# Performance work log

Hardware: AMD Instinct MI355X
Metric: run time of the kernel (lower is better)

## Reference

```python
import jax, jax.numpy as jnp
import numpy as np

B, F, S = 8, 4000, 512   # batch, input_size, seq_len
E = H = 128              # embedding_size == hidden_size (linearlist applied to embedded nodes)
TOPK = 8
USE_MASK = True
EPS = 1e-4


def setup_inputs() -> dict:
    key = jax.random.key(0)
    k1, k2, k3, k4, k5 = jax.random.split(key, 5)
    be = 1.0 / np.sqrt(E)
    bh = 1.0 / np.sqrt(H)
    inputs = jax.random.uniform(k1, (B, F, S), dtype=jnp.float32)
    embedding = jax.random.uniform(k2, (F, E), minval=-be, maxval=be, dtype=jnp.float32)
    # stacked nn.ModuleList of seq_len Linear(hidden_size, seq_len) layers
    W = jax.random.uniform(k3, (S, H, S), minval=-bh, maxval=bh, dtype=jnp.float32)
    b = jax.random.uniform(k4, (S, S), minval=-bh, maxval=bh, dtype=jnp.float32)
    offset_prob = jax.random.uniform(k5, (1,), dtype=jnp.float32)  # unused by forward
    return {"inputs": inputs, "embedding": embedding, "W": W, "b": b, "offset_prob": offset_prob}


def _probs(inputs, embedding, W, b):
    # GraphEmbedding: tanh(inputs[:, :, i]^T @ embedding) for each node i -> [B,S,E]
    embedded = jnp.tanh(jnp.einsum('bfs,fe->bse', inputs, embedding))
    # per-node linear: logits[b, i, :] = embedded[b, i, :] @ W[i] + b[i]
    logits = jnp.einsum('bih,iho->bio', embedded, W) + b[None]
    return jnp.clip(jax.nn.sigmoid(logits), EPS, 1.0 - EPS)  # [B,S,S], == prev_probs


def _select_and_mask(probs):
    """Sequential per-node edge sampling + acyclic (transitive-closure) mask update.

    mask[b, a, c] == True  <=>  a is an ancestor of c in the DAG built so far.
    Vectorized equivalent of compute_mask/mask propagation in the torch source.
    """
    keys = jax.random.split(jax.random.key(42), S)
    batch_ix = jnp.arange(B)[:, None]

    def step(mask, xs):
        idx, key, p = xs  # p: [B, S] probabilities for node idx's parents
        samp = jax.random.bernoulli(key, p)  # [B, S] bool
        if TOPK != 0:
            _, top_ids = jax.lax.top_k(p, TOPK)
            keep = jnp.zeros((B, S), bool).at[batch_ix, top_ids].set(True)
            samp = samp & keep
        if USE_MASK:
            # apply_mask_to_actions: cannot pick a descendant of idx as parent
            samp = samp & ~mask[:, idx, :]
        samp = samp.at[:, idx].set(False)  # no self loop
        if USE_MASK:
            # compute_mask: add edges j->idx for selected j, keep transitive closure
            anc_of_sel = jnp.any(mask & samp[:, None, :], axis=-1)   # ancestors of any selected j
            col = mask[:, :, idx] | samp | anc_of_sel                # new ancestors of idx
            mask = mask.at[:, :, idx].set(col)
            row = mask[:, idx, :]                                    # descendants of idx
            mask = mask | (col[:, :, None] & row[:, None, :])        # anc(idx) x desc(idx)
        return mask, samp

    mask0 = jnp.zeros((B, S, S), bool)
    p_steps = jnp.transpose(probs, (1, 0, 2))  # [S, B, S]
    mask, rows = jax.lax.scan(step, mask0, (jnp.arange(S), keys, p_steps))
    prev_idxs = jnp.transpose(rows, (1, 0, 2))  # [B, S, S]
    return prev_idxs, mask


def reference(inputs, embedding, W, b, offset_prob):
    prev_probs = _probs(inputs, embedding, W, b)
    prev_idxs, mask = _select_and_mask(prev_probs)
    prev_probs_2 = jnp.zeros_like(prev_probs)  # never written in the torch forward
    return prev_probs, prev_probs_2, prev_idxs, mask
```

## Files before the change

kernel.cpp:

```cpp
#include <hip/hip_runtime.h>
#include <stdint.h>

#define S_    512
#define B_    8
#define F_    4000
#define E_    128
#define H_    128
#define TOPK_ 8
#define S2_   (S_*S_)
#define BSS_  (B_*S2_)
#define BSE_  (B_*S_*E_)
#define NCHUNK_ 8
typedef unsigned long long ull;

__device__ __forceinline__ void tf2x32(uint32_t k0, uint32_t k1, uint32_t& x0, uint32_t& x1) {
  uint32_t k2 = k0 ^ k1 ^ 0x1BD11BDAu;
  x0 += k0; x1 += k1;
#define TFR(r) { x0 += x1; x1 = (x1 << (r)) | (x1 >> (32 - (r))); x1 ^= x0; }
  TFR(13) TFR(15) TFR(26) TFR(6)
  x0 += k1; x1 += k2 + 1u;
  TFR(17) TFR(29) TFR(16) TFR(24)
  x0 += k2; x1 += k0 + 2u;
  TFR(13) TFR(15) TFR(26) TFR(6)
  x0 += k0; x1 += k1 + 3u;
  TFR(17) TFR(29) TFR(16) TFR(24)
  x0 += k1; x1 += k2 + 4u;
  TFR(13) TFR(15) TFR(26) TFR(6)
  x0 += k2; x1 += k0 + 5u;
#undef TFR
}

__device__ __forceinline__ void splitkey(int i, uint32_t& k0, uint32_t& k1) {
  uint32_t x0 = 0u, x1 = (uint32_t)i;
  tf2x32(0u, 42u, x0, x1);
  k0 = x0; k1 = x1;
}
__device__ __forceinline__ uint32_t randbits32(uint32_t k0, uint32_t k1, uint32_t m) {
  uint32_t x0 = 0u, x1 = m;
  tf2x32(k0, k1, x0, x1);
  return x0 ^ x1;
}

__global__ __launch_bounds__(256) void embed_kernel(const float* __restrict__ inputs,
                                                    const float* __restrict__ embedding,
                                                    double* __restrict__ part) {
  const int c  = blockIdx.x >> 7;
  const int b  = (blockIdx.x >> 4) & 7;
  const int s0 = (blockIdx.x & 15) << 5;
  const int fbeg = c << 9;
  const int fend = (fbeg + 512 < F_) ? fbeg + 512 : F_;
  const int t  = threadIdx.x;
  const int sl = t >> 4;
  const int eg = t & 15;
  __shared__ float inA[16][32];
  double acc0[8], acc1[8];
#pragma unroll
  for (int j = 0; j < 8; j++) { acc0[j] = 0.0; acc1[j] = 0.0; }
  const int lr = t >> 4, lc = t & 15;
  for (int f0 = fbeg; f0 < fend; f0 += 16) {
    __syncthreads();
    const float* ip = inputs + (size_t)(b*F_ + f0 + lr)*S_ + s0 + lc;
    inA[lr][lc]      = ip[0];
    inA[lr][lc + 16] = ip[16];
    __syncthreads();
#pragma unroll
    for (int k = 0; k < 16; k++) {
      double a0 = (double)inA[k][sl];
      double a1 = (double)inA[k][sl + 16];
      const float4* ep = (const float4*)(embedding + (size_t)(f0 + k)*E_ + eg*8);
      float4 w0 = ep[0], w1 = ep[1];
      double wd0 = (double)w0.x, wd1 = (double)w0.y, wd2 = (double)w0.z, wd3 = (double)w0.w;
      double wd4 = (double)w1.x, wd5 = (double)w1.y, wd6 = (double)w1.z, wd7 = (double)w1.w;
      acc0[0] += a0*wd0; acc0[1] += a0*wd1; acc0[2] += a0*wd2; acc0[3] += a0*wd3;
      acc0[4] += a0*wd4; acc0[5] += a0*wd5; acc0[6] += a0*wd6; acc0[7] += a0*wd7;
      acc1[0] += a1*wd0; acc1[1] += a1*wd1; acc1[2] += a1*wd2; acc1[3] += a1*wd3;
      acc1[4] += a1*wd4; acc1[5] += a1*wd5; acc1[6] += a1*wd6; acc1[7] += a1*wd7;
    }
  }
  double* op0 = part + (size_t)c*BSE_ + (size_t)(b*S_ + s0 + sl)*E_ + eg*8;
  double* op1 = op0 + 16*E_;
#pragma unroll
  for (int j = 0; j < 8; j++) { op0[j] = acc0[j]; op1[j] = acc1[j]; }
}

__global__ __launch_bounds__(256) void reduce_tanh_kernel(float* __restrict__ outbase) {
  const size_t j = (size_t)blockIdx.x*256 + threadIdx.x;
  const double* part = (const double*)outbase;
  double s = 0.0;
#pragma unroll
  for (int c = 0; c < NCHUNK_; c++) s += part[(size_t)c*BSE_ + j];
  double* emb64 = (double*)(outbase + 3*(size_t)BSS_);
  emb64[j] = tanh(s);
}

__global__ __launch_bounds__(256) void logits_kernel(const double* __restrict__ emb64,
                                                     const float* __restrict__ W,
                                                     const float* __restrict__ bias,
                                                     double* __restrict__ p64,
                                                     float* __restrict__ p32) {
  const int i  = blockIdx.x >> 3;
  const int o0 = (blockIdx.x & 7) << 6;
  const int t  = threadIdx.x;
  const int o  = o0 + (t & 63);
  const int bg = t >> 6;
  __shared__ double eL[8][128];
#pragma unroll
  for (int k = 0; k < 4; k++) {
    int q = t + k*256;
    eL[q >> 7][q & 127] = emb64[(size_t)((q >> 7)*S_ + i)*E_ + (q & 127)];
  }
  __syncthreads();
  double a0 = 0.0, a1 = 0.0;
  const float* Wp = W + (size_t)i*H_*S_ + o;
  for (int h = 0; h < H_; h++) {
    double w = (double)Wp[(size_t)h*S_];
    a0 += eL[bg][h]     * w;
    a1 += eL[bg + 4][h] * w;
  }
  double bd = (double)bias[i*S_ + o];
  double q0 = 1.0 / (1.0 + exp(-(a0 + bd)));
  double q1 = 1.0 / (1.0 + exp(-(a1 + bd)));
  q0 = fmin(fmax(q0, 1e-4), 1.0 - 1e-4);
  q1 = fmin(fmax(q1, 1e-4), 1.0 - 1e-4);
  size_t i0 = (size_t)(bg*S_ + i)*S_ + o;
  size_t i1 = (size_t)((bg + 4)*S_ + i)*S_ + o;
  p64[i0] = q0; p64[i1] = q1;
  p32[i0] = (float)q0; p32[i1] = (float)q1;
}

__global__ __launch_bounds__(64) void samppre_kernel(const double* __restrict__ p64,
                                                     float* __restrict__ outbase) {
  const int i = blockIdx.x >> 3;
  const int b = blockIdx.x & 7;
  const int l = threadIdx.x;
  ull* samp_pre = (ull*)(outbase + 3*(size_t)BSS_ + (size_t)b*S2_);
  uint32_t k0, k1;
  splitkey(i, k0, k1);
  double pv[8]; bool sb[8]; bool usedk[8]; bool keep[8];
#pragma unroll
  for (int w = 0; w < 8; w++) {
    int c = (w << 6) + l;
    uint32_t m = (uint32_t)(b*S_ + c);
    uint32_t bits = randbits32(k0, k1, m);
    float uf = __uint_as_float((bits >> 9) | 0x3f800000u) - 1.0f;
    double p = p64[(size_t)(b*S_ + i)*S_ + c];
    pv[w] = p;
    sb[w] = ((double)uf < p) && (c != i);
    usedk[w] = false; keep[w] = false;
  }
  for (int r = 0; r < TOPK_; r++) {
    double bp = -1.0; int bc = 0x7fffffff;
#pragma unroll
    for (int w = 0; w < 8; w++) {
      int c = (w << 6) + l;
      if (!usedk[w] && (pv[w] > bp || (pv[w] == bp && c < bc))) { bp = pv[w]; bc = c; }
    }
#pragma unroll
    for (int d = 1; d < 64; d <<= 1) {
      double op = __shfl_xor(bp, d);
      int    oc = __shfl_xor(bc, d);
      if (op > bp || (op == bp && oc < bc)) { bp = op; bc = oc; }
    }
    if ((bc & 63) == l) { usedk[bc >> 6] = true; keep[bc >> 6] = true; }
  }
#pragma unroll
  for (int w = 0; w < 8; w++) {
    ull word = __ballot((int)(sb[w] && keep[w]));
    if (l == 0) samp_pre[i*8 + w] = word;
  }
}

__global__ __launch_bounds__(512, 1) void scan_kernel(float* __restrict__ outbase) {
  const int b  = blockIdx.x;
  const int wv = threadIdx.x >> 6;
  const int l  = threadIdx.x & 63;
  const ull* __restrict__ samp_pre = (const ull*)(outbase + 3*(size_t)BSS_ + (size_t)b*S2_);
  ull* sampPack = (ull*)(outbase + (size_t)BSS_) + (size_t)b*8192;
  ull* Dpack    = sampPack + 4096;

  __shared__ ull spreL[4096];
  __shared__ ull rowbuf[2][8];
  for (int q = threadIdx.x; q < 4096; q += 512) spreL[q] = samp_pre[q];
  if (threadIdx.x < 16) ((ull*)rowbuf)[threadIdx.x] = 0ULL;
  ull Dw[8];
#pragma unroll
  for (int w = 0; w < 8; w++) Dw[w] = 0ULL;
  __syncthreads();

  ull pre_cur[8];
#pragma unroll
  for (int w = 0; w < 8; w++) pre_cur[w] = spreL[w];
  ull pre_v = spreL[wv];

#pragma unroll
  for (int iw = 0; iw < 8; iw++) {
    for (int ib = 0; ib < 64; ib++) {
      const int idx  = (iw << 6) + ib;
      const int nidx = (idx + 1) & (S_ - 1);
      const int niw  = nidx >> 6, nib = nidx & 63;
      ull pre_nxt[8];
#pragma unroll
      for (int w = 0; w < 8; w++) pre_nxt[w] = spreL[(nidx << 3) + w];
      ull pre_v_nxt = spreL[(nidx << 3) + wv];

      ull row[8];
#pragma unroll
      for (int w = 0; w < 8; w++) row[w] = rowbuf[idx & 1][w];
      ull row_v = rowbuf[idx & 1][wv];
      ull sw[8];
#pragma unroll
      for (int w = 0; w < 8; w++) sw[w] = pre_cur[w] & ~row[w];
      const ull swv = pre_v & ~row_v;
      if (wv == 0) {
        ull myw = sw[0];
#pragma unroll
        for (int w = 1; w < 8; w++) myw = (l == w) ? sw[w] : myw;
        if (l < 8) sampPack[(idx << 3) + l] = myw;
      }
      const ull ibit = 1ULL << ib;
      ull t = Dw[iw] & ibit;
#pragma unroll
      for (int w = 0; w < 8; w++) {
        if (sw[w] != 0ULL) t |= Dw[w] & sw[w];
      }
      const ull col = __ballot((int)(t != 0ULL)) | swv;
      if (col != 0ULL) {
        const ull m   = 0ULL - ((col >> l) & 1ULL);
        const ull riw = row[iw] | ibit;
#pragma unroll
        for (int w = 0; w < 8; w++) Dw[w] |= ((w == iw) ? riw : row[w]) & m;
      }
      if (wv == niw && l == nib) {
#pragma unroll
        for (int w = 0; w < 8; w++) rowbuf[nidx & 1][w] = Dw[w];
      }
      __syncthreads();
#pragma unroll
      for (int w = 0; w < 8; w++) pre_cur[w] = pre_nxt[w];
      pre_v = pre_v_nxt;
    }
  }
#pragma unroll
  for (int w = 0; w < 8; w++)
    Dpack[(((wv << 3) + w) << 6) + l] = Dw[w];
}

__global__ __launch_bounds__(256) void expand_kernel(float* __restrict__ outbase) {
  const ull* pack = (const ull*)(outbase + (size_t)BSS_);
  unsigned int tid = blockIdx.x*256 + threadIdx.x;
  const unsigned int half = 1u << 18;
  if (tid < half) {
    unsigned int t = tid;
    int b = t >> 15, tin = t & 32767, r = tin >> 6, cg = tin & 63;
    ull word = pack[(size_t)b*8192 + (r << 3) + (cg >> 3)];
    int sh = (cg & 7) << 3;
    float* dst = outbase + 2*(size_t)BSS_ + ((size_t)b << 18) + (r << 9) + (cg << 3);
    float4 v0 = make_float4((float)((word >> (sh+0)) & 1ULL), (float)((word >> (sh+1)) & 1ULL),
                            (float)((word >> (sh+2)) & 1ULL), (float)((word >> (sh+3)) & 1ULL));
    float4 v1 = make_float4((float)((word >> (sh+4)) & 1ULL), (float)((word >> (sh+5)) & 1ULL),
                            (float)((word >> (sh+6)) & 1ULL), (float)((word >> (sh+7)) & 1ULL));
    ((float4*)dst)[0] = v0; ((float4*)dst)[1] = v1;
  } else {
    unsigned int t = tid - half;
    int b = t >> 15, tin = t & 32767, a = tin >> 6, cg = tin & 63;
    const ull* Dp = pack + (size_t)b*8192 + 4096;
    ull word = Dp[((((a >> 6) << 3) + (cg >> 3)) << 6) + (a & 63)];
    int sh = (cg & 7) << 3;
    float* dst = outbase + 3*(size_t)BSS_ + ((size_t)b << 18) + (a << 9) + (cg << 3);
    float4 v0 = make_float4((float)((word >> (sh+0)) & 1ULL), (float)((word >> (sh+1)) & 1ULL),
                            (float)((word >> (sh+2)) & 1ULL), (float)((word >> (sh+3)) & 1ULL));
    float4 v1 = make_float4((float)((word >> (sh+4)) & 1ULL), (float)((word >> (sh+5)) & 1ULL),
                            (float)((word >> (sh+6)) & 1ULL), (float)((word >> (sh+7)) & 1ULL));
    ((float4*)dst)[0] = v0; ((float4*)dst)[1] = v1;
  }
}

extern "C" void kernel_launch(void* const* d_in, const int* in_sizes, int n_in,
                              void* d_out, int out_size, void* d_ws, size_t ws_size,
                              hipStream_t stream) {
  const float* inputs    = (const float*)d_in[0];
  const float* embedding = (const float*)d_in[1];
  const float* W         = (const float*)d_in[2];
  const float* bias      = (const float*)d_in[3];
  float* out = (float*)d_out;
  double* part  = (double*)out;
  double* emb64 = (double*)(out + 3*(size_t)BSS_);
  double* p64   = (double*)(out + (size_t)BSS_);

  embed_kernel      <<<1024, 256, 0, stream>>>(inputs, embedding, part);
  reduce_tanh_kernel<<<2048, 256, 0, stream>>>(out);
  logits_kernel     <<<4096, 256, 0, stream>>>(emb64, W, bias, p64, out);
  samppre_kernel    <<<4096, 64,  0, stream>>>(p64, out);
  scan_kernel       <<<8,    512, 0, stream>>>(out);
  expand_kernel     <<<2048, 256, 0, stream>>>(out);
  hipMemsetAsync(out + (size_t)BSS_, 0, (size_t)BSS_ * sizeof(float), stream);
}
```

Baseline: 545.4 us.

## Widen embed tile to 64 nodes and streamline the scan loop body

The embedding GEMM kernel now computes 64 sequence positions per block instead of 32, so each thread holds four accumulator sets and reuses every loaded embedding value across twice as many rows, with half as many blocks launched. Separately, the sequential scan drops its register prefetch of the next step's sample words and reads them from LDS directly. It also skips OR updates for zero row words and moves the sampPack store after the mask update, shortening the serial critical path. The trade-off is higher register pressure in the fp64 embed kernel, which may cut occupancy, and LDS reads now sit on the scan's dependency chain.

```diff
diff --git a/kernel.cpp b/kernel.cpp
--- a/kernel.cpp
+++ b/kernel.cpp
@@ -44,29 +44,33 @@
 __global__ __launch_bounds__(256) void embed_kernel(const float* __restrict__ inputs,
                                                     const float* __restrict__ embedding,
                                                     double* __restrict__ part) {
-  const int c  = blockIdx.x >> 7;
-  const int b  = (blockIdx.x >> 4) & 7;
-  const int s0 = (blockIdx.x & 15) << 5;
+  const int c  = blockIdx.x >> 6;
+  const int b  = (blockIdx.x >> 3) & 7;
+  const int s0 = (blockIdx.x & 7) << 6;
   const int fbeg = c << 9;
   const int fend = (fbeg + 512 < F_) ? fbeg + 512 : F_;
   const int t  = threadIdx.x;
   const int sl = t >> 4;
   const int eg = t & 15;
-  __shared__ float inA[16][32];
-  double acc0[8], acc1[8];
-#pragma unroll
-  for (int j = 0; j < 8; j++) { acc0[j] = 0.0; acc1[j] = 0.0; }
+  __shared__ float inA[16][64];
+  double acc0[8], acc1[8], acc2[8], acc3[8];
+#pragma unroll
+  for (int j = 0; j < 8; j++) { acc0[j] = 0.0; acc1[j] = 0.0; acc2[j] = 0.0; acc3[j] = 0.0; }
   const int lr = t >> 4, lc = t & 15;
   for (int f0 = fbeg; f0 < fend; f0 += 16) {
     __syncthreads();
     const float* ip = inputs + (size_t)(b*F_ + f0 + lr)*S_ + s0 + lc;
     inA[lr][lc]      = ip[0];
     inA[lr][lc + 16] = ip[16];
+    inA[lr][lc + 32] = ip[32];
+    inA[lr][lc + 48] = ip[48];
     __syncthreads();
 #pragma unroll
     for (int k = 0; k < 16; k++) {
       double a0 = (double)inA[k][sl];
       double a1 = (double)inA[k][sl + 16];
+      double a2 = (double)inA[k][sl + 32];
+      double a3 = (double)inA[k][sl + 48];
       const float4* ep = (const float4*)(embedding + (size_t)(f0 + k)*E_ + eg*8);
       float4 w0 = ep[0], w1 = ep[1];
       double wd0 = (double)w0.x, wd1 = (double)w0.y, wd2 = (double)w0.z, wd3 = (double)w0.w;
@@ -75,12 +79,18 @@
       acc0[4] += a0*wd4; acc0[5] += a0*wd5; acc0[6] += a0*wd6; acc0[7] += a0*wd7;
       acc1[0] += a1*wd0; acc1[1] += a1*wd1; acc1[2] += a1*wd2; acc1[3] += a1*wd3;
       acc1[4] += a1*wd4; acc1[5] += a1*wd5; acc1[6] += a1*wd6; acc1[7] += a1*wd7;
+      acc2[0] += a2*wd0; acc2[1] += a2*wd1; acc2[2] += a2*wd2; acc2[3] += a2*wd3;
+      acc2[4] += a2*wd4; acc2[5] += a2*wd5; acc2[6] += a2*wd6; acc2[7] += a2*wd7;
+      acc3[0] += a3*wd0; acc3[1] += a3*wd1; acc3[2] += a3*wd2; acc3[3] += a3*wd3;
+      acc3[4] += a3*wd4; acc3[5] += a3*wd5; acc3[6] += a3*wd6; acc3[7] += a3*wd7;
     }
   }
   double* op0 = part + (size_t)c*BSE_ + (size_t)(b*S_ + s0 + sl)*E_ + eg*8;
   double* op1 = op0 + 16*E_;
-#pragma unroll
-  for (int j = 0; j < 8; j++) { op0[j] = acc0[j]; op1[j] = acc1[j]; }
+  double* op2 = op0 + 32*E_;
+  double* op3 = op0 + 48*E_;
+#pragma unroll
+  for (int j = 0; j < 8; j++) { op0[j] = acc0[j]; op1[j] = acc1[j]; op2[j] = acc2[j]; op3[j] = acc3[j]; }
 }
 
 __global__ __launch_bounds__(256) void reduce_tanh_kernel(float* __restrict__ outbase) {
@@ -187,57 +197,47 @@
   for (int w = 0; w < 8; w++) Dw[w] = 0ULL;
   __syncthreads();
 
-  ull pre_cur[8];
-#pragma unroll
-  for (int w = 0; w < 8; w++) pre_cur[w] = spreL[w];
-  ull pre_v = spreL[wv];
-
 #pragma unroll
   for (int iw = 0; iw < 8; iw++) {
     for (int ib = 0; ib < 64; ib++) {
       const int idx  = (iw << 6) + ib;
       const int nidx = (idx + 1) & (S_ - 1);
       const int niw  = nidx >> 6, nib = nidx & 63;
-      ull pre_nxt[8];
-#pragma unroll
-      for (int w = 0; w < 8; w++) pre_nxt[w] = spreL[(nidx << 3) + w];
-      ull pre_v_nxt = spreL[(nidx << 3) + wv];
-
       ull row[8];
 #pragma unroll
       for (int w = 0; w < 8; w++) row[w] = rowbuf[idx & 1][w];
-      ull row_v = rowbuf[idx & 1][wv];
+      const ull row_v = rowbuf[idx & 1][wv];
+      const ull pre_v = spreL[(idx << 3) + wv];
       ull sw[8];
 #pragma unroll
-      for (int w = 0; w < 8; w++) sw[w] = pre_cur[w] & ~row[w];
+      for (int w = 0; w < 8; w++) sw[w] = spreL[(idx << 3) + w] & ~row[w];
       const ull swv = pre_v & ~row_v;
+      const ull ibit = 1ULL << ib;
+      ull t = Dw[iw] & ibit;
+#pragma unroll
+      for (int w = 0; w < 8; w++) {
+        if (sw[w] != 0ULL) t |= Dw[w] & sw[w];
+      }
+      const ull col = __ballot((int)(t != 0ULL)) | swv;
+      if (col != 0ULL) {
+        const ull m = 0ULL - ((col >> l) & 1ULL);
+        Dw[iw] |= (row[iw] | ibit) & m;
+#pragma unroll
+        for (int w = 0; w < 8; w++) {
+          if (w != iw && row[w] != 0ULL) Dw[w] |= row[w] & m;
+        }
+      }
+      if (wv == niw && l == nib) {
+#pragma unroll
+        for (int w = 0; w < 8; w++) rowbuf[nidx & 1][w] = Dw[w];
+      }
       if (wv == 0) {
         ull myw = sw[0];
 #pragma unroll
         for (int w = 1; w < 8; w++) myw = (l == w) ? sw[w] : myw;
         if (l < 8) sampPack[(idx << 3) + l] = myw;
       }
-      const ull ibit = 1ULL << ib;
-      ull t = Dw[iw] & ibit;
-#pragma unroll
-      for (int w = 0; w < 8; w++) {
-        if (sw[w] != 0ULL) t |= Dw[w] & sw[w];
-      }
-      const ull col = __ballot((int)(t != 0ULL)) | swv;
-      if (col != 0ULL) {
-        const ull m   = 0ULL - ((col >> l) & 1ULL);
-        const ull riw = row[iw] | ibit;
-#pragma unroll
-        for (int w = 0; w < 8; w++) Dw[w] |= ((w == iw) ? riw : row[w]) & m;
-      }
-      if (wv == niw && l == nib) {
-#pragma unroll
-        for (int w = 0; w < 8; w++) rowbuf[nidx & 1][w] = Dw[w];
-      }
       __syncthreads();
-#pragma unroll
-      for (int w = 0; w < 8; w++) pre_cur[w] = pre_nxt[w];
-      pre_v = pre_v_nxt;
     }
   }
 #pragma unroll
@@ -287,7 +287,7 @@
   double* emb64 = (double*)(out + 3*(size_t)BSS_);
   double* p64   = (double*)(out + (size_t)BSS_);
 
-  embed_kernel      <<<1024, 256, 0, stream>>>(inputs, embedding, part);
+  embed_kernel      <<<512,  256, 0, stream>>>(inputs, embedding, part);
   reduce_tanh_kernel<<<2048, 256, 0, stream>>>(out);
   logits_kernel     <<<4096, 256, 0, stream>>>(emb64, W, bias, p64, out);
   samppre_kernel    <<<4096, 64,  0, stream>>>(p64, out);
```

Result: slower. 600.5 us (+10.1%).
